# Kernel tuning notes

Hardware: AMD Instinct MI355X
Metric: run time of the kernel (lower is better)

Reference implementation:

```python
import jax, jax.numpy as jnp
import numpy as np

TAU = 100.0
EPS = 1e-6

def _norm(a):
    n = jnp.linalg.norm(a, axis=-1, keepdims=True)
    return a / jnp.maximum(n, EPS)

def setup_inputs() -> dict:
    key = jax.random.key(0)
    k1, k2, k3 = jax.random.split(key, 3)
    A, T, B, V, D = 64, 32, 64, 12, 512
    text_feat = jax.random.normal(k1, (A, T, D), dtype=jnp.float32)
    video_feat = jax.random.normal(k2, (B, V, D), dtype=jnp.float32)
    text_mask = jax.random.randint(k3, (A, T), 0, 2, dtype=jnp.int32)
    # guarantee at least one valid token per text so masked softmaxes are finite
    text_mask = text_mask.at[:, 0].set(1)
    return {"text_feat": text_feat, "video_feat": video_feat, "text_mask": text_mask}

def reference(text_feat, video_feat, text_mask):
    tm = text_mask.astype(text_feat.dtype)          # [A,T]
    t = _norm(text_feat)                            # [A,T,D]
    v = _norm(video_feat)                           # [B,V,D]
    neg_inf = jnp.asarray(-jnp.inf, t.dtype)

    logits = jnp.einsum('atd,bvd->abtv', t, v)      # [A,B,T,V]
    logits = logits * tm[:, None, :, None]          # zero out masked text tokens

    # video-side softmax over frames v, then aggregate video into text space
    vps1 = jax.nn.softmax(logits * TAU, axis=-1)            # [A,B,T,V]
    tf1 = jnp.einsum('abtv,bvd->abtd', vps1, v)             # [A,B,T,D]  (largest intermediate)
    t2v = jnp.einsum('abtd,atd->abt', tf1, t)               # [A,B,T]

    # text-side masked softmax over tokens t, aggregate text into video space
    tps1 = jax.nn.softmax(jnp.where(logits == 0, neg_inf, logits) * TAU, axis=-2)
    vf1 = jnp.einsum('abtv,atd->abvd', tps1, t)             # [A,B,V,D]
    v2t = jnp.einsum('abvd,bvd->abv', vf1, v)               # [A,B,V]

    tps2 = jax.nn.softmax(jnp.where(t2v == 0, neg_inf, t2v) * TAU, axis=-1)
    vf2 = jnp.einsum('abt,atd->abd', tps2, t)               # [A,B,D]
    vps2 = jax.nn.softmax(v2t * TAU, axis=-1)
    tf2 = jnp.einsum('abv,bvd->abd', vps2, v)               # [A,B,D]

    return jnp.einsum('abd,abd->ab', vf2, tf2)              # [A,B]
```

## Files before the change

### kernel.cpp

```cpp
#include <hip/hip_runtime.h>
#include <math.h>

#define A_ 64
#define T_ 32
#define B_ 64
#define V_ 12
#define D_ 512
#define TAUF 100.0f
#define NCH 8

#define AHI 0
#define ALO 8192
#define BHI 16384
#define BLO 22528
#define BUFBYTES 28672

typedef __attribute__((ext_vector_type(8))) short bf16x8;
typedef __attribute__((ext_vector_type(4))) float f32x4;

__device__ __forceinline__ void splitT(const float4 x0, const float4 x1,
                                       bf16x8& hv, bf16x8& lv, float& ss)
{
    float y[8] = {x0.x, x0.y, x0.z, x0.w, x1.x, x1.y, x1.z, x1.w};
    #pragma unroll
    for (int j = 0; j < 8; ++j) {
        ss += y[j] * y[j];
        unsigned int u = __float_as_uint(y[j]);
        float hf = __uint_as_float(u & 0xffff0000u);
        hv[j] = (short)(u >> 16);
        lv[j] = (short)(__float_as_uint(y[j] - hf) >> 16);
    }
}

__global__ __launch_bounds__(256)
void fused_kernel(const float* __restrict__ text,
                  const float* __restrict__ video,
                  const int* __restrict__ mask,
                  float* __restrict__ out)
{
    const int wgid = blockIdx.x;
    const int xcd  = wgid & 7;
    const int i    = wgid >> 3;
    const int bm   = xcd * 4 + (i >> 4);
    const int bn   = i & 15;
    const int tid  = threadIdx.x;
    const int wid  = tid >> 6;
    const int lane = tid & 63;
    const int r16  = lane & 15;
    const int kg4  = lane >> 4;

    __shared__ __align__(16) char stage[2][BUFBYTES];
    __shared__ float nrmA[8][64];
    __shared__ float nrmB[8][48];
    __shared__ float invA[64];
    __shared__ float invB[48];
    __shared__ int   msh[2][T_];
    __shared__ float v2t_sh[8][V_];
    __shared__ float wv_sh[8][V_];
    __shared__ float stats1[8];

    if (tid < 64) msh[tid >> 5][tid & 31] = mask[(bm * 2 + (tid >> 5)) * T_ + (tid & 31)];

    const int arow0 = tid >> 3, akg = tid & 7;
    const int arow1 = arow0 + 32;
    const float* asrc0 = text + ((size_t)(bm * 64 + arow0)) * D_ + akg * 8;
    const float* asrc1 = text + ((size_t)(bm * 64 + arow1)) * D_ + akg * 8;
    const int brow0 = tid >> 3, bkg = tid & 7;
    const int brow1 = brow0 + 24;
    const float* bsrc0 = video + ((size_t)(bn * 48 + brow0)) * D_ + bkg * 8;
    const float* bsrc1 = video + ((size_t)(bn * 48 + brow1)) * D_ + bkg * 8;

    const int adst0 = (akg * 64 + (arow0 ^ akg)) * 16;
    const int adst1 = (akg * 64 + (arow1 ^ akg)) * 16;
    const int bdst0 = BHI + (bkg * 48 + (brow0 ^ bkg)) * 16;
    const int bdst1 = BHI + (bkg * 48 + (brow1 ^ bkg)) * 16;

    float ssA0 = 0.f, ssA1 = 0.f, ssB0 = 0.f, ssB1 = 0.f;

    auto PACK = [&](int bufi, int k) {
        char* buf = stage[bufi];
        {
            const float4* s = (const float4*)(asrc0 + k * 64);
            bf16x8 hv, lv;
            splitT(s[0], s[1], hv, lv, ssA0);
            *(bf16x8*)(buf + adst0)       = hv;
            *(bf16x8*)(buf + ALO + adst0) = lv;
        }
        {
            const float4* s = (const float4*)(asrc1 + k * 64);
            bf16x8 hv, lv;
            splitT(s[0], s[1], hv, lv, ssA1);
            *(bf16x8*)(buf + adst1)       = hv;
            *(bf16x8*)(buf + ALO + adst1) = lv;
        }
        if (tid < 192) {
            {
                const float4* s = (const float4*)(bsrc0 + k * 64);
                bf16x8 hv, lv;
                splitT(s[0], s[1], hv, lv, ssB0);
                *(bf16x8*)(buf + bdst0)             = hv;
                *(bf16x8*)(buf + (BLO - BHI) + bdst0) = lv;
            }
            {
                const float4* s = (const float4*)(bsrc1 + k * 64);
                bf16x8 hv, lv;
                splitT(s[0], s[1], hv, lv, ssB1);
                *(bf16x8*)(buf + bdst1)             = hv;
                *(bf16x8*)(buf + (BLO - BHI) + bdst1) = lv;
            }
        }
    };

    const int rowa = wid * 16 + r16;
    int aoff[2], boff[2][3];
    #pragma unroll
    for (int s = 0; s < 2; ++s) {
        int kg = s * 4 + kg4;
        aoff[s] = (kg * 64 + (rowa ^ kg)) * 16;
        #pragma unroll
        for (int c = 0; c < 3; ++c) {
            int rowb = c * 16 + r16;
            boff[s][c] = BHI + (kg * 48 + (rowb ^ kg)) * 16;
        }
    }

    f32x4 acc0 = {0.f, 0.f, 0.f, 0.f};
    f32x4 acc1 = {0.f, 0.f, 0.f, 0.f};
    f32x4 acc2 = {0.f, 0.f, 0.f, 0.f};

    PACK(0, 0);
    __syncthreads();

    #pragma unroll 2
    for (int k = 0; k < NCH; ++k) {
        if (k + 1 < NCH) PACK((k + 1) & 1, k + 1);
        const char* buf = stage[k & 1];
        #pragma unroll
        for (int s = 0; s < 2; ++s) {
            bf16x8 aH  = *(const bf16x8*)(buf + aoff[s]);
            bf16x8 aL  = *(const bf16x8*)(buf + ALO + aoff[s]);
            bf16x8 bH0 = *(const bf16x8*)(buf + boff[s][0]);
            bf16x8 bL0 = *(const bf16x8*)(buf + (BLO - BHI) + boff[s][0]);
            bf16x8 bH1 = *(const bf16x8*)(buf + boff[s][1]);
            bf16x8 bL1 = *(const bf16x8*)(buf + (BLO - BHI) + boff[s][1]);
            bf16x8 bH2 = *(const bf16x8*)(buf + boff[s][2]);
            bf16x8 bL2 = *(const bf16x8*)(buf + (BLO - BHI) + boff[s][2]);
            acc0 = __builtin_amdgcn_mfma_f32_16x16x32_bf16(aH, bH0, acc0, 0, 0, 0);
            acc1 = __builtin_amdgcn_mfma_f32_16x16x32_bf16(aH, bH1, acc1, 0, 0, 0);
            acc2 = __builtin_amdgcn_mfma_f32_16x16x32_bf16(aH, bH2, acc2, 0, 0, 0);
            acc0 = __builtin_amdgcn_mfma_f32_16x16x32_bf16(aH, bL0, acc0, 0, 0, 0);
            acc1 = __builtin_amdgcn_mfma_f32_16x16x32_bf16(aH, bL1, acc1, 0, 0, 0);
            acc2 = __builtin_amdgcn_mfma_f32_16x16x32_bf16(aH, bL2, acc2, 0, 0, 0);
            acc0 = __builtin_amdgcn_mfma_f32_16x16x32_bf16(aL, bH0, acc0, 0, 0, 0);
            acc1 = __builtin_amdgcn_mfma_f32_16x16x32_bf16(aL, bH1, acc1, 0, 0, 0);
            acc2 = __builtin_amdgcn_mfma_f32_16x16x32_bf16(aL, bH2, acc2, 0, 0, 0);
        }
        __syncthreads();
    }

    nrmA[akg][arow0] = ssA0;
    nrmA[akg][arow1] = ssA1;
    if (tid < 192) { nrmB[bkg][brow0] = ssB0; nrmB[bkg][brow1] = ssB1; }
    __syncthreads();
    if (tid < 64) {
        float s = 0.f;
        #pragma unroll
        for (int j = 0; j < 8; ++j) s += nrmA[j][tid];
        invA[tid] = 1.0f / fmaxf(sqrtf(s), 1e-6f);
    } else if (tid < 112) {
        int r = tid - 64;
        float s = 0.f;
        #pragma unroll
        for (int j = 0; j < 8; ++j) s += nrmB[j][r];
        invB[r] = 1.0f / fmaxf(sqrtf(s), 1e-6f);
    }
    __syncthreads();

    float* Lf = (float*)&stage[0][0];
    {
        #pragma unroll
        for (int r = 0; r < 4; ++r) {
            int Mrow0 = wid * 16 + kg4 * 4 + r;
            int al = Mrow0 >> 5, t = Mrow0 & 31;
            float ia = invA[Mrow0];
            int c0 = r16, c1 = 16 + r16, c2 = 32 + r16;
            int bl0 = c0 / 12, bl1 = c1 / 12, bl2 = c2 / 12;
            Lf[((al * 4 + bl0) * T_ + t) * V_ + (c0 - bl0 * 12)] = acc0[r] * ia * invB[c0];
            Lf[((al * 4 + bl1) * T_ + t) * V_ + (c1 - bl1 * 12)] = acc1[r] * ia * invB[c1];
            Lf[((al * 4 + bl2) * T_ + t) * V_ + (c2 - bl2 * 12)] = acc2[r] * ia * invB[c2];
        }
    }
    __syncthreads();

    const int p   = tid >> 5;
    const int l32 = tid & 31;
    const int al  = p >> 2, bl = p & 3;
    const float* Lrow = &Lf[((al * 4 + bl) * T_ + l32) * V_];

    float t2v_val;
    {
        float l[V_];
        #pragma unroll
        for (int j = 0; j < V_; ++j) l[j] = Lrow[j];
        if (msh[al][l32]) {
            float m = -1e30f;
            #pragma unroll
            for (int j = 0; j < V_; ++j) m = fmaxf(m, l[j]);
            float s = 0.f, num = 0.f;
            #pragma unroll
            for (int j = 0; j < V_; ++j) {
                float e = expf(TAUF * (l[j] - m));
                s += e; num += e * l[j];
            }
            t2v_val = num / s;
        } else {
            float s = 0.f;
            #pragma unroll
            for (int j = 0; j < V_; ++j) s += l[j];
            t2v_val = s * (1.0f / V_);
        }
    }

    bool  ex = (t2v_val == 0.0f);
    float xm = ex ? -1e30f : t2v_val;
    #pragma unroll
    for (int m = 16; m >= 1; m >>= 1) xm = fmaxf(xm, __shfl_xor(xm, m, 32));
    float w2 = ex ? 0.0f : expf(TAUF * (t2v_val - xm));
    float W2 = w2;
    #pragma unroll
    for (int m = 16; m >= 1; m >>= 1) W2 += __shfl_xor(W2, m, 32);

    if (l32 < V_) {
        float m = -1e30f;
        for (int j = 0; j < T_; ++j) {
            float Lraw = Lf[((al * 4 + bl) * T_ + j) * V_ + l32];
            float Lm = msh[al][j] ? Lraw : 0.0f;
            if (Lm != 0.0f) m = fmaxf(m, Lm);
        }
        float s = 0.f, num = 0.f;
        for (int j = 0; j < T_; ++j) {
            float Lraw = Lf[((al * 4 + bl) * T_ + j) * V_ + l32];
            float Lm = msh[al][j] ? Lraw : 0.0f;
            if (Lm != 0.0f) {
                float e = expf(TAUF * (Lm - m));
                s += e; num += e * Lraw;
            }
        }
        v2t_sh[p][l32] = num / s;
    }
    __syncthreads();

    if (l32 < V_) {
        float m = -1e30f;
        #pragma unroll
        for (int j = 0; j < V_; ++j) m = fmaxf(m, v2t_sh[p][j]);
        float s = 0.f;
        #pragma unroll
        for (int j = 0; j < V_; ++j) s += expf(TAUF * (v2t_sh[p][j] - m));
        wv_sh[p][l32] = expf(TAUF * (v2t_sh[p][l32] - m));
        if (l32 == 0) stats1[p] = s;
    }
    __syncthreads();

    {
        float pD = 0.f;
        #pragma unroll
        for (int j = 0; j < V_; ++j) pD += wv_sh[p][j] * Lrow[j];
        pD *= w2;
        #pragma unroll
        for (int m = 16; m >= 1; m >>= 1) pD += __shfl_xor(pD, m, 32);
        if (l32 == 0)
            out[(bm * 2 + al) * B_ + bn * 4 + bl] = pD / (W2 * stats1[p]);
    }
}

extern "C" void kernel_launch(void* const* d_in, const int* in_sizes, int n_in,
                              void* d_out, int out_size, void* d_ws, size_t ws_size,
                              hipStream_t stream) {
    const float* text  = (const float*)d_in[0];
    const float* video = (const float*)d_in[1];
    const int*   mask  = (const int*)d_in[2];
    float* out = (float*)d_out;

    fused_kernel<<<512, 256, 0, stream>>>(text, video, mask, out);
}
```

Baseline: 20.69 us.

## Single-buffer LDS staging with register prefetch and occupancy hint

Replaces the LDS double-buffer with a single staging buffer. Each chunk's global loads are now issued into registers before the MFMA work, and the bf16 hi/lo split and LDS write happen after a barrier. This halves the staging LDS and adds a launch-bounds hint of 4 blocks per CU, aiming for more resident workgroups. In exchange it adds an extra barrier per chunk and serialises the split/write with compute instead of overlapping them.

```diff
diff --git a/kernel.cpp b/kernel.cpp
--- a/kernel.cpp
+++ b/kernel.cpp
@@ -32,7 +32,7 @@
     }
 }
 
-__global__ __launch_bounds__(256)
+__global__ __launch_bounds__(256, 4)
 void fused_kernel(const float* __restrict__ text,
                   const float* __restrict__ video,
                   const int* __restrict__ mask,
@@ -49,7 +49,7 @@
     const int r16  = lane & 15;
     const int kg4  = lane >> 4;
 
-    __shared__ __align__(16) char stage[2][BUFBYTES];
+    __shared__ __align__(16) char stage[BUFBYTES];
     __shared__ float nrmA[8][64];
     __shared__ float nrmB[8][48];
     __shared__ float invA[64];
@@ -77,37 +77,35 @@
 
     float ssA0 = 0.f, ssA1 = 0.f, ssB0 = 0.f, ssB1 = 0.f;
 
-    auto PACK = [&](int bufi, int k) {
-        char* buf = stage[bufi];
-        {
-            const float4* s = (const float4*)(asrc0 + k * 64);
-            bf16x8 hv, lv;
-            splitT(s[0], s[1], hv, lv, ssA0);
-            *(bf16x8*)(buf + adst0)       = hv;
-            *(bf16x8*)(buf + ALO + adst0) = lv;
-        }
-        {
-            const float4* s = (const float4*)(asrc1 + k * 64);
-            bf16x8 hv, lv;
-            splitT(s[0], s[1], hv, lv, ssA1);
-            *(bf16x8*)(buf + adst1)       = hv;
-            *(bf16x8*)(buf + ALO + adst1) = lv;
-        }
+    float4 ra0[2], ra1[2], rb0[2], rb1[2];
+
+    auto LOAD = [&](int k) {
+        const float4* s0 = (const float4*)(asrc0 + k * 64);
+        const float4* s1 = (const float4*)(asrc1 + k * 64);
+        ra0[0] = s0[0]; ra0[1] = s0[1];
+        ra1[0] = s1[0]; ra1[1] = s1[1];
         if (tid < 192) {
-            {
-                const float4* s = (const float4*)(bsrc0 + k * 64);
-                bf16x8 hv, lv;
-                splitT(s[0], s[1], hv, lv, ssB0);
-                *(bf16x8*)(buf + bdst0)             = hv;
-                *(bf16x8*)(buf + (BLO - BHI) + bdst0) = lv;
-            }
-            {
-                const float4* s = (const float4*)(bsrc1 + k * 64);
-                bf16x8 hv, lv;
-                splitT(s[0], s[1], hv, lv, ssB1);
-                *(bf16x8*)(buf + bdst1)             = hv;
-                *(bf16x8*)(buf + (BLO - BHI) + bdst1) = lv;
-            }
+            const float4* t0 = (const float4*)(bsrc0 + k * 64);
+            const float4* t1 = (const float4*)(bsrc1 + k * 64);
+            rb0[0] = t0[0]; rb0[1] = t0[1];
+            rb1[0] = t1[0]; rb1[1] = t1[1];
+        }
+    };
+    auto WRITE = [&]() {
+        bf16x8 hv, lv;
+        splitT(ra0[0], ra0[1], hv, lv, ssA0);
+        *(bf16x8*)(stage + adst0)       = hv;
+        *(bf16x8*)(stage + ALO + adst0) = lv;
+        splitT(ra1[0], ra1[1], hv, lv, ssA1);
+        *(bf16x8*)(stage + adst1)       = hv;
+        *(bf16x8*)(stage + ALO + adst1) = lv;
+        if (tid < 192) {
+            splitT(rb0[0], rb0[1], hv, lv, ssB0);
+            *(bf16x8*)(stage + bdst0)               = hv;
+            *(bf16x8*)(stage + (BLO - BHI) + bdst0) = lv;
+            splitT(rb1[0], rb1[1], hv, lv, ssB1);
+            *(bf16x8*)(stage + bdst1)               = hv;
+            *(bf16x8*)(stage + (BLO - BHI) + bdst1) = lv;
         }
     };
 
@@ -128,23 +126,23 @@
     f32x4 acc1 = {0.f, 0.f, 0.f, 0.f};
     f32x4 acc2 = {0.f, 0.f, 0.f, 0.f};
 
-    PACK(0, 0);
+    LOAD(0);
+    WRITE();
     __syncthreads();
 
     #pragma unroll 2
     for (int k = 0; k < NCH; ++k) {
-        if (k + 1 < NCH) PACK((k + 1) & 1, k + 1);
-        const char* buf = stage[k & 1];
+        if (k + 1 < NCH) LOAD(k + 1);
         #pragma unroll
         for (int s = 0; s < 2; ++s) {
-            bf16x8 aH  = *(const bf16x8*)(buf + aoff[s]);
-            bf16x8 aL  = *(const bf16x8*)(buf + ALO + aoff[s]);
-            bf16x8 bH0 = *(const bf16x8*)(buf + boff[s][0]);
-            bf16x8 bL0 = *(const bf16x8*)(buf + (BLO - BHI) + boff[s][0]);
-            bf16x8 bH1 = *(const bf16x8*)(buf + boff[s][1]);
-            bf16x8 bL1 = *(const bf16x8*)(buf + (BLO - BHI) + boff[s][1]);
-            bf16x8 bH2 = *(const bf16x8*)(buf + boff[s][2]);
-            bf16x8 bL2 = *(const bf16x8*)(buf + (BLO - BHI) + boff[s][2]);
+            bf16x8 aH  = *(const bf16x8*)(stage + aoff[s]);
+            bf16x8 aL  = *(const bf16x8*)(stage + ALO + aoff[s]);
+            bf16x8 bH0 = *(const bf16x8*)(stage + boff[s][0]);
+            bf16x8 bL0 = *(const bf16x8*)(stage + (BLO - BHI) + boff[s][0]);
+            bf16x8 bH1 = *(const bf16x8*)(stage + boff[s][1]);
+            bf16x8 bL1 = *(const bf16x8*)(stage + (BLO - BHI) + boff[s][1]);
+            bf16x8 bH2 = *(const bf16x8*)(stage + boff[s][2]);
+            bf16x8 bL2 = *(const bf16x8*)(stage + (BLO - BHI) + boff[s][2]);
             acc0 = __builtin_amdgcn_mfma_f32_16x16x32_bf16(aH, bH0, acc0, 0, 0, 0);
             acc1 = __builtin_amdgcn_mfma_f32_16x16x32_bf16(aH, bH1, acc1, 0, 0, 0);
             acc2 = __builtin_amdgcn_mfma_f32_16x16x32_bf16(aH, bH2, acc2, 0, 0, 0);
@@ -156,6 +154,10 @@
             acc2 = __builtin_amdgcn_mfma_f32_16x16x32_bf16(aL, bH2, acc2, 0, 0, 0);
         }
         __syncthreads();
+        if (k + 1 < NCH) {
+            WRITE();
+            __syncthreads();
+        }
     }
 
     nrmA[akg][arow0] = ssA0;
@@ -176,7 +178,7 @@
     }
     __syncthreads();
 
-    float* Lf = (float*)&stage[0][0];
+    float* Lf = (float*)&stage[0];
     {
         #pragma unroll
         for (int r = 0; r < 4; ++r) {
```

Result: slower. 22.43 us (+8.4%).

## Prefetch global chunks two stages ahead into registers, split load from LDS write

Applied to the files above, without the earlier changes.

Splits the combined load-and-pack step into a register-prefetch LOAD and a later split-and-store WRITE. Global loads for chunk k+2 are issued before the MFMAs of chunk k, and chunk k+1 is written to shared memory after them, so global latency overlaps compute. The main loop is also fully unrolled. The cost is two register sets of prefetched floats (up to 16 float4 per thread), which raises VGPR pressure and may lower occupancy.

```diff
diff --git a/kernel.cpp b/kernel.cpp
--- a/kernel.cpp
+++ b/kernel.cpp
@@ -9,7 +9,6 @@
 #define TAUF 100.0f
 #define NCH 8
 
-#define AHI 0
 #define ALO 8192
 #define BHI 16384
 #define BLO 22528
@@ -31,6 +30,8 @@
         lv[j] = (short)(__float_as_uint(y[j] - hf) >> 16);
     }
 }
+
+struct RegSet { float4 a0[2], a1[2], b0[2], b1[2]; };
 
 __global__ __launch_bounds__(256)
 void fused_kernel(const float* __restrict__ text,
@@ -77,37 +78,36 @@
 
     float ssA0 = 0.f, ssA1 = 0.f, ssB0 = 0.f, ssB1 = 0.f;
 
-    auto PACK = [&](int bufi, int k) {
+    RegSet rs0, rs1;
+
+    auto LOAD = [&](RegSet& R, int k) {
+        const float4* s0 = (const float4*)(asrc0 + k * 64);
+        const float4* s1 = (const float4*)(asrc1 + k * 64);
+        R.a0[0] = s0[0]; R.a0[1] = s0[1];
+        R.a1[0] = s1[0]; R.a1[1] = s1[1];
+        if (tid < 192) {
+            const float4* t0 = (const float4*)(bsrc0 + k * 64);
+            const float4* t1 = (const float4*)(bsrc1 + k * 64);
+            R.b0[0] = t0[0]; R.b0[1] = t0[1];
+            R.b1[0] = t1[0]; R.b1[1] = t1[1];
+        }
+    };
+    auto WRITE = [&](RegSet& R, int bufi) {
         char* buf = stage[bufi];
-        {
-            const float4* s = (const float4*)(asrc0 + k * 64);
-            bf16x8 hv, lv;
-            splitT(s[0], s[1], hv, lv, ssA0);
-            *(bf16x8*)(buf + adst0)       = hv;
-            *(bf16x8*)(buf + ALO + adst0) = lv;
-        }
-        {
-            const float4* s = (const float4*)(asrc1 + k * 64);
-            bf16x8 hv, lv;
-            splitT(s[0], s[1], hv, lv, ssA1);
-            *(bf16x8*)(buf + adst1)       = hv;
-            *(bf16x8*)(buf + ALO + adst1) = lv;
-        }
+        bf16x8 hv, lv;
+        splitT(R.a0[0], R.a0[1], hv, lv, ssA0);
+        *(bf16x8*)(buf + adst0)       = hv;
+        *(bf16x8*)(buf + ALO + adst0) = lv;
+        splitT(R.a1[0], R.a1[1], hv, lv, ssA1);
+        *(bf16x8*)(buf + adst1)       = hv;
+        *(bf16x8*)(buf + ALO + adst1) = lv;
         if (tid < 192) {
-            {
-                const float4* s = (const float4*)(bsrc0 + k * 64);
-                bf16x8 hv, lv;
-                splitT(s[0], s[1], hv, lv, ssB0);
-                *(bf16x8*)(buf + bdst0)             = hv;
-                *(bf16x8*)(buf + (BLO - BHI) + bdst0) = lv;
-            }
-            {
-                const float4* s = (const float4*)(bsrc1 + k * 64);
-                bf16x8 hv, lv;
-                splitT(s[0], s[1], hv, lv, ssB1);
-                *(bf16x8*)(buf + bdst1)             = hv;
-                *(bf16x8*)(buf + (BLO - BHI) + bdst1) = lv;
-            }
+            splitT(R.b0[0], R.b0[1], hv, lv, ssB0);
+            *(bf16x8*)(buf + bdst0)               = hv;
+            *(bf16x8*)(buf + (BLO - BHI) + bdst0) = lv;
+            splitT(R.b1[0], R.b1[1], hv, lv, ssB1);
+            *(bf16x8*)(buf + bdst1)               = hv;
+            *(bf16x8*)(buf + (BLO - BHI) + bdst1) = lv;
         }
     };
 
@@ -128,12 +128,14 @@
     f32x4 acc1 = {0.f, 0.f, 0.f, 0.f};
     f32x4 acc2 = {0.f, 0.f, 0.f, 0.f};
 
-    PACK(0, 0);
-    __syncthreads();
-
-    #pragma unroll 2
+    LOAD(rs0, 0);
+    WRITE(rs0, 0);
+    LOAD(rs1, 1);
+    __syncthreads();
+
+    #pragma unroll
     for (int k = 0; k < NCH; ++k) {
-        if (k + 1 < NCH) PACK((k + 1) & 1, k + 1);
+        if (k + 2 < NCH) LOAD((k & 1) ? rs1 : rs0, k + 2);
         const char* buf = stage[k & 1];
         #pragma unroll
         for (int s = 0; s < 2; ++s) {
@@ -155,6 +157,7 @@
             acc1 = __builtin_amdgcn_mfma_f32_16x16x32_bf16(aL, bH1, acc1, 0, 0, 0);
             acc2 = __builtin_amdgcn_mfma_f32_16x16x32_bf16(aL, bH2, acc2, 0, 0, 0);
         }
+        if (k + 1 < NCH) WRITE((k & 1) ? rs0 : rs1, (k + 1) & 1);
         __syncthreads();
     }
 
```

After: 20.80 us. Within noise of the previous version (+0.5%).

## Load A fragments directly into registers and prefetch two chunks ahead

Applied to the files above, without the earlier changes.

Each wave now loads its own text rows straight from global memory into registers and splits them into bf16 hi/lo MFMA fragments there, so the text tile no longer passes through shared memory. Global loads for both operands are issued two chunks ahead, and the split/write of the next chunk happens after the current MFMAs so load latency overlaps compute. The text norm is reduced with wave shuffles instead of a shared-memory array. This shrinks the LDS staging buffer and removes the A-side LDS traffic, at the cost of more live registers and uncoalesced-per-wave row loads.

```diff
diff --git a/kernel.cpp b/kernel.cpp
--- a/kernel.cpp
+++ b/kernel.cpp
@@ -9,11 +9,8 @@
 #define TAUF 100.0f
 #define NCH 8
 
-#define AHI 0
-#define ALO 8192
-#define BHI 16384
-#define BLO 22528
-#define BUFBYTES 28672
+#define BLO 6144
+#define BUFBYTES 12288
 
 typedef __attribute__((ext_vector_type(8))) short bf16x8;
 typedef __attribute__((ext_vector_type(4))) float f32x4;
@@ -31,6 +28,10 @@
         lv[j] = (short)(__float_as_uint(y[j] - hf) >> 16);
     }
 }
+
+struct ARegs { float4 r[4]; };
+struct BRegs { float4 r[4]; };
+struct AFrag { bf16x8 h[2], l[2]; };
 
 __global__ __launch_bounds__(256)
 void fused_kernel(const float* __restrict__ text,
@@ -50,7 +51,6 @@
     const int kg4  = lane >> 4;
 
     __shared__ __align__(16) char stage[2][BUFBYTES];
-    __shared__ float nrmA[8][64];
     __shared__ float nrmB[8][48];
     __shared__ float invA[64];
     __shared__ float invB[48];
@@ -61,66 +61,60 @@
 
     if (tid < 64) msh[tid >> 5][tid & 31] = mask[(bm * 2 + (tid >> 5)) * T_ + (tid & 31)];
 
-    const int arow0 = tid >> 3, akg = tid & 7;
-    const int arow1 = arow0 + 32;
-    const float* asrc0 = text + ((size_t)(bm * 64 + arow0)) * D_ + akg * 8;
-    const float* asrc1 = text + ((size_t)(bm * 64 + arow1)) * D_ + akg * 8;
+    const float* aptr = text + ((size_t)(bm * 64 + wid * 16 + r16)) * D_ + kg4 * 8;
+
     const int brow0 = tid >> 3, bkg = tid & 7;
     const int brow1 = brow0 + 24;
     const float* bsrc0 = video + ((size_t)(bn * 48 + brow0)) * D_ + bkg * 8;
     const float* bsrc1 = video + ((size_t)(bn * 48 + brow1)) * D_ + bkg * 8;
-
-    const int adst0 = (akg * 64 + (arow0 ^ akg)) * 16;
-    const int adst1 = (akg * 64 + (arow1 ^ akg)) * 16;
-    const int bdst0 = BHI + (bkg * 48 + (brow0 ^ bkg)) * 16;
-    const int bdst1 = BHI + (bkg * 48 + (brow1 ^ bkg)) * 16;
-
-    float ssA0 = 0.f, ssA1 = 0.f, ssB0 = 0.f, ssB1 = 0.f;
-
-    auto PACK = [&](int bufi, int k) {
-        char* buf = stage[bufi];
-        {
-            const float4* s = (const float4*)(asrc0 + k * 64);
+    const int bdst0 = (bkg * 48 + (brow0 ^ bkg)) * 16;
+    const int bdst1 = (bkg * 48 + (brow1 ^ bkg)) * 16;
+
+    float ssA = 0.f, ssB0 = 0.f, ssB1 = 0.f;
+
+    ARegs ra0, ra1;
+    BRegs rb0, rb1;
+    AFrag fa0, fa1;
+
+    auto LOADA = [&](ARegs& R, int k) {
+        const float4* p0 = (const float4*)(aptr + k * 64);
+        const float4* p1 = (const float4*)(aptr + k * 64 + 32);
+        R.r[0] = p0[0]; R.r[1] = p0[1];
+        R.r[2] = p1[0]; R.r[3] = p1[1];
+    };
+    auto LOADB = [&](BRegs& R, int k) {
+        if (tid < 192) {
+            const float4* t0 = (const float4*)(bsrc0 + k * 64);
+            const float4* t1 = (const float4*)(bsrc1 + k * 64);
+            R.r[0] = t0[0]; R.r[1] = t0[1];
+            R.r[2] = t1[0]; R.r[3] = t1[1];
+        }
+    };
+    auto SPLITA = [&](ARegs& R, AFrag& F) {
+        splitT(R.r[0], R.r[1], F.h[0], F.l[0], ssA);
+        splitT(R.r[2], R.r[3], F.h[1], F.l[1], ssA);
+    };
+    auto WRITEB = [&](BRegs& R, int bufi) {
+        if (tid < 192) {
+            char* buf = stage[bufi];
             bf16x8 hv, lv;
-            splitT(s[0], s[1], hv, lv, ssA0);
-            *(bf16x8*)(buf + adst0)       = hv;
-            *(bf16x8*)(buf + ALO + adst0) = lv;
-        }
-        {
-            const float4* s = (const float4*)(asrc1 + k * 64);
-            bf16x8 hv, lv;
-            splitT(s[0], s[1], hv, lv, ssA1);
-            *(bf16x8*)(buf + adst1)       = hv;
-            *(bf16x8*)(buf + ALO + adst1) = lv;
-        }
-        if (tid < 192) {
-            {
-                const float4* s = (const float4*)(bsrc0 + k * 64);
-                bf16x8 hv, lv;
-                splitT(s[0], s[1], hv, lv, ssB0);
-                *(bf16x8*)(buf + bdst0)             = hv;
-                *(bf16x8*)(buf + (BLO - BHI) + bdst0) = lv;
-            }
-            {
-                const float4* s = (const float4*)(bsrc1 + k * 64);
-                bf16x8 hv, lv;
-                splitT(s[0], s[1], hv, lv, ssB1);
-                *(bf16x8*)(buf + bdst1)             = hv;
-                *(bf16x8*)(buf + (BLO - BHI) + bdst1) = lv;
-            }
-        }
-    };
-
-    const int rowa = wid * 16 + r16;
-    int aoff[2], boff[2][3];
+            splitT(R.r[0], R.r[1], hv, lv, ssB0);
+            *(bf16x8*)(buf + bdst0)       = hv;
+            *(bf16x8*)(buf + BLO + bdst0) = lv;
+            splitT(R.r[2], R.r[3], hv, lv, ssB1);
+            *(bf16x8*)(buf + bdst1)       = hv;
+            *(bf16x8*)(buf + BLO + bdst1) = lv;
+        }
+    };
+
+    int boff[2][3];
     #pragma unroll
     for (int s = 0; s < 2; ++s) {
         int kg = s * 4 + kg4;
-        aoff[s] = (kg * 64 + (rowa ^ kg)) * 16;
         #pragma unroll
         for (int c = 0; c < 3; ++c) {
             int rowb = c * 16 + r16;
-            boff[s][c] = BHI + (kg * 48 + (rowb ^ kg)) * 16;
+            boff[s][c] = (kg * 48 + (rowb ^ kg)) * 16;
         }
     }
 
@@ -128,23 +122,30 @@
     f32x4 acc1 = {0.f, 0.f, 0.f, 0.f};
     f32x4 acc2 = {0.f, 0.f, 0.f, 0.f};
 
-    PACK(0, 0);
-    __syncthreads();
-
-    #pragma unroll 2
+    LOADA(ra0, 0);  LOADB(rb0, 0);
+    SPLITA(ra0, fa0);
+    WRITEB(rb0, 0);
+    LOADA(ra1, 1);  LOADB(rb1, 1);
+    __syncthreads();
+
+    #pragma unroll
     for (int k = 0; k < NCH; ++k) {
-        if (k + 1 < NCH) PACK((k + 1) & 1, k + 1);
+        if (k + 2 < NCH) {
+            LOADA((k & 1) ? ra1 : ra0, k + 2);
+            LOADB((k & 1) ? rb1 : rb0, k + 2);
+        }
+        const AFrag& fc = (k & 1) ? fa1 : fa0;
         const char* buf = stage[k & 1];
         #pragma unroll
         for (int s = 0; s < 2; ++s) {
-            bf16x8 aH  = *(const bf16x8*)(buf + aoff[s]);
-            bf16x8 aL  = *(const bf16x8*)(buf + ALO + aoff[s]);
+            bf16x8 aH  = fc.h[s];
+            bf16x8 aL  = fc.l[s];
             bf16x8 bH0 = *(const bf16x8*)(buf + boff[s][0]);
-            bf16x8 bL0 = *(const bf16x8*)(buf + (BLO - BHI) + boff[s][0]);
+            bf16x8 bL0 = *(const bf16x8*)(buf + BLO + boff[s][0]);
             bf16x8 bH1 = *(const bf16x8*)(buf + boff[s][1]);
-            bf16x8 bL1 = *(const bf16x8*)(buf + (BLO - BHI) + boff[s][1]);
+            bf16x8 bL1 = *(const bf16x8*)(buf + BLO + boff[s][1]);
             bf16x8 bH2 = *(const bf16x8*)(buf + boff[s][2]);
-            bf16x8 bL2 = *(const bf16x8*)(buf + (BLO - BHI) + boff[s][2]);
+            bf16x8 bL2 = *(const bf16x8*)(buf + BLO + boff[s][2]);
             acc0 = __builtin_amdgcn_mfma_f32_16x16x32_bf16(aH, bH0, acc0, 0, 0, 0);
             acc1 = __builtin_amdgcn_mfma_f32_16x16x32_bf16(aH, bH1, acc1, 0, 0, 0);
             acc2 = __builtin_amdgcn_mfma_f32_16x16x32_bf16(aH, bH2, acc2, 0, 0, 0);
@@ -155,24 +156,26 @@
             acc1 = __builtin_amdgcn_mfma_f32_16x16x32_bf16(aL, bH1, acc1, 0, 0, 0);
             acc2 = __builtin_amdgcn_mfma_f32_16x16x32_bf16(aL, bH2, acc2, 0, 0, 0);
         }
+        if (k + 1 < NCH) {
+            SPLITA((k & 1) ? ra0 : ra1, (k & 1) ? fa0 : fa1);
+            WRITEB((k & 1) ? rb0 : rb1, (k + 1) & 1);
+        }
         __syncthreads();
     }
 
-    nrmA[akg][arow0] = ssA0;
-    nrmA[akg][arow1] = ssA1;
+    {
+        float sA = ssA;
+        sA += __shfl_xor(sA, 16);
+        sA += __shfl_xor(sA, 32);
+        if (kg4 == 0) invA[wid * 16 + r16] = 1.0f / fmaxf(sqrtf(sA), 1e-6f);
+    }
     if (tid < 192) { nrmB[bkg][brow0] = ssB0; nrmB[bkg][brow1] = ssB1; }
     __syncthreads();
-    if (tid < 64) {
+    if (tid < 48) {
         float s = 0.f;
         #pragma unroll
-        for (int j = 0; j < 8; ++j) s += nrmA[j][tid];
-        invA[tid] = 1.0f / fmaxf(sqrtf(s), 1e-6f);
-    } else if (tid < 112) {
-        int r = tid - 64;
-        float s = 0.f;
-        #pragma unroll
-        for (int j = 0; j < 8; ++j) s += nrmB[j][r];
-        invB[r] = 1.0f / fmaxf(sqrtf(s), 1e-6f);
+        for (int j = 0; j < 8; ++j) s += nrmB[j][tid];
+        invB[tid] = 1.0f / fmaxf(sqrtf(s), 1e-6f);
     }
     __syncthreads();
 
```

New measurement: 23.54 us. +13.8%, slower.
